# Kernel tuning notes

Measured on AMD Instinct MI355X. Metric: run time of the kernel, lower is better.

## Reference

```python
import jax, jax.numpy as jnp
import numpy as np

N, E = 4096, 4096          # nodes, hyperedges
IN_DIM, OUT_DIM, EDGE_DIM = 256, 256, 64
HEADS, DEG, CARD = 8, 8, 8  # node degree, edge cardinality (regular hypergraph)


def setup_inputs() -> dict:
    key = jax.random.key(0)
    ks = jax.random.split(key, 6)
    # regular hypergraph: DEG rounds, each a permutation of nodes chunked into
    # blocks of CARD -> every node in exactly DEG edges, every edge has CARD
    # distinct nodes. E = DEG * N / CARD.
    rng = np.random.default_rng(0)
    node_of_edge = np.concatenate(
        [rng.permutation(N).reshape(-1, CARD) for _ in range(DEG)], axis=0)  # [E, CARD]
    inc = np.zeros((E, N), dtype=np.float32)
    inc[np.arange(E)[:, None], node_of_edge] = 1.0
    s = 0.05
    return {
        "x": jax.random.normal(ks[0], (N, IN_DIM), jnp.float32),
        "incidence": jnp.asarray(inc),
        "edge_attr": jax.random.normal(ks[1], (E, EDGE_DIM), jnp.float32),
        "W_lin": jax.random.normal(ks[2], (IN_DIM, OUT_DIM), jnp.float32) * s,
        "W_edge": jax.random.normal(ks[3], (EDGE_DIM, OUT_DIM), jnp.float32) * s,
        "in_proj_w": jax.random.normal(ks[4], (3 * OUT_DIM, OUT_DIM), jnp.float32) * s,
        "in_proj_b": jnp.zeros((3 * OUT_DIM,), jnp.float32),
        "out_proj_w": jax.random.normal(ks[5], (OUT_DIM, OUT_DIM), jnp.float32) * s,
        "out_proj_b": jnp.zeros((OUT_DIM,), jnp.float32),
        "deg": DEG,
        "card": CARD,
    }


def reference(x, incidence, edge_attr, W_lin, W_edge,
              in_proj_w, in_proj_b, out_proj_w, out_proj_b, deg, card):
    n = x.shape[0]
    Wh = x @ W_lin          # [N, D]
    We = edge_attr @ W_edge  # [E, D]
    Dm = Wh.shape[1]
    H = HEADS
    dh = Dm // H
    # recover regular structure from the binary incidence matrix.
    # (attention is permutation-invariant over the pair set, so the order of
    #  indices returned by top_k vs torch.nonzero does not matter)
    _, edge_of_node = jax.lax.top_k(incidence.T, deg)   # [N, deg]
    _, node_of_edge = jax.lax.top_k(incidence, card)    # [E, card]
    pair_e = edge_of_node[:, :, None]                   # [N, deg, 1]
    pair_u = node_of_edge[edge_of_node]                 # [N, deg, card]
    L = deg * card
    Ksrc = (Wh[pair_u] + We[pair_e]).reshape(n, L, Dm)  # key source per pair
    Vsrc = Wh[pair_u].reshape(n, L, Dm)                 # value source per pair
    # torch nn.MultiheadAttention in/out projections
    Wq, Wk, Wv = jnp.split(in_proj_w, 3, axis=0)
    bq, bk, bv = jnp.split(in_proj_b, 3)
    q = (Wh @ Wq.T + bq).reshape(n, H, dh)              # q_len = 1 per node
    k = (Ksrc @ Wk.T + bk).reshape(n, L, H, dh)
    v = (Vsrc @ Wv.T + bv).reshape(n, L, H, dh)
    scale = 1.0 / jnp.sqrt(jnp.asarray(dh, q.dtype))
    scores = jnp.einsum('nhd,nlhd->nhl', q, k) * scale  # [N, H, L]
    attn = jax.nn.softmax(scores, axis=-1)
    ctx = jnp.einsum('nhl,nlhd->nhd', attn, v).reshape(n, Dm)
    out = ctx @ out_proj_w.T + out_proj_b
    return jax.nn.relu(out)
```

## Files before the change

### kernel.cpp

```cpp
#include <hip/hip_runtime.h>
#include <hip/hip_bf16.h>

#define NN    4096
#define EE    4096
#define DM    256
#define EDIM  64
#define HH    8
#define DHd   32
#define LL    64

typedef short  s16x8 __attribute__((ext_vector_type(8)));
typedef unsigned short u16x8 __attribute__((ext_vector_type(8)));
typedef float  f32x4 __attribute__((ext_vector_type(4)));
typedef unsigned int u32x4v __attribute__((ext_vector_type(4)));

#define SCALE 0.17677669529663687f

__device__ __forceinline__ float b2f(unsigned short u) {
  return __uint_as_float(((unsigned int)u) << 16);
}
__device__ __forceinline__ unsigned short f2b_bits(float f) {
  unsigned int u = __float_as_uint(f);
  u = (u + 0x7FFFu + ((u >> 16) & 1u)) >> 16;
  return (unsigned short)u;
}

#if __has_builtin(__builtin_amdgcn_fdot2_f32_bf16)
#define HAVE_DOT2B 1
typedef __bf16 bf2v __attribute__((ext_vector_type(2)));
__device__ __forceinline__ float dot2b(unsigned int a, unsigned int b, float c) {
  return __builtin_amdgcn_fdot2_f32_bf16(__builtin_bit_cast(bf2v, a),
                                         __builtin_bit_cast(bf2v, b), c, false);
}
#else
#define HAVE_DOT2B 0
#endif

#if __has_builtin(__builtin_amdgcn_update_dpp) && __has_builtin(__builtin_amdgcn_readfirstlane)
#define HAVE_DPP 1
template <int CTRL>
__device__ __forceinline__ float dpp_sum_step(float x) {
  int s = __builtin_amdgcn_update_dpp(0, __float_as_int(x), CTRL, 0xF, 0xF, true);
  return x + __int_as_float(s);
}
#else
#define HAVE_DPP 0
#endif

#define MODE_PLAIN 0
#define MODE_PROJ  1
#define MODE_OUT   2

__device__ __forceinline__ void gemm_mfma_body(
    short* As, short* Bs, f32x4 acc[2][2], int wr, int wc, int fr, int fk) {
  s16x8 af0 = *(const s16x8*)&As[(wr + fr) * 40 + fk];
  s16x8 af1 = *(const s16x8*)&As[(wr + 16 + fr) * 40 + fk];
  s16x8 bf0 = *(const s16x8*)&Bs[(wc + fr) * 40 + fk];
  s16x8 bf1 = *(const s16x8*)&Bs[(wc + 16 + fr) * 40 + fk];
  acc[0][0] = __builtin_amdgcn_mfma_f32_16x16x32_bf16(af0, bf0, acc[0][0], 0, 0, 0);
  acc[0][1] = __builtin_amdgcn_mfma_f32_16x16x32_bf16(af0, bf1, acc[0][1], 0, 0, 0);
  acc[1][0] = __builtin_amdgcn_mfma_f32_16x16x32_bf16(af1, bf0, acc[1][0], 0, 0, 0);
  acc[1][1] = __builtin_amdgcn_mfma_f32_16x16x32_bf16(af1, bf1, acc[1][1], 0, 0, 0);
}

__device__ __forceinline__ void gemm_tile(
    const unsigned short* __restrict__ A, const unsigned short* __restrict__ B,
    int i0, int j0, int N, int K, int mode,
    float* __restrict__ out_f, unsigned short* __restrict__ out_b,
    unsigned short* __restrict__ out_b2, const float* __restrict__ bias,
    short* As, short* Bs) {
  const int tid  = threadIdx.x;
  const int wid  = tid >> 6, lane = tid & 63;
  const int wr   = (wid >> 1) * 32, wc = (wid & 1) * 32;
  const int srow = tid >> 2, schunk = (tid & 3) * 8;
  const int fr   = lane & 15, fk = (lane >> 4) * 8;

  f32x4 acc[2][2];
#pragma unroll
  for (int a = 0; a < 2; ++a)
#pragma unroll
    for (int b = 0; b < 2; ++b) acc[a][b] = (f32x4){0.f, 0.f, 0.f, 0.f};

  for (int kk = 0; kk < K; kk += 32) {
    *(s16x8*)&As[srow * 40 + schunk] = *(const s16x8*)&A[(size_t)(i0 + srow) * K + kk + schunk];
    *(s16x8*)&Bs[srow * 40 + schunk] = *(const s16x8*)&B[(size_t)(j0 + srow) * K + kk + schunk];
    __syncthreads();
    gemm_mfma_body(As, Bs, acc, wr, wc, fr, fk);
    __syncthreads();
  }

  const int ecol = lane & 15, erow0 = (lane >> 4) * 4;
#pragma unroll
  for (int mi = 0; mi < 2; ++mi)
#pragma unroll
    for (int ni = 0; ni < 2; ++ni) {
#pragma unroll
      for (int v = 0; v < 4; ++v) {
        int i = i0 + wr + mi * 16 + erow0 + v;
        int j = j0 + wc + ni * 16 + ecol;
        float val = acc[mi][ni][v];
        if (mode == MODE_PLAIN) {
          out_b[(size_t)i * N + j] = f2b_bits(val);
        } else if (mode == MODE_PROJ) {
          if (j < 256)      out_b[(size_t)i * 256 + j]           = f2b_bits((val + bias[j]) * SCALE);
          else if (j < 512) out_b2[(size_t)i * 256 + (j - 256)]  = f2b_bits(val);
          else              ((unsigned short*)out_f)[(size_t)i * 256 + (j - 512)] = f2b_bits(val + bias[j]);
        } else {
          float r = val + bias[j];
          out_f[(size_t)i * N + j] = r > 0.f ? r : 0.f;
        }
      }
    }
}

__device__ __forceinline__ void gemm_tile_f32src(
    const float* __restrict__ A, const float* __restrict__ B,
    int i0, int j0, int N, int K,
    unsigned short* __restrict__ out_b, short* As, short* Bs) {
  const int tid  = threadIdx.x;
  const int wid  = tid >> 6, lane = tid & 63;
  const int wr   = (wid >> 1) * 32, wc = (wid & 1) * 32;
  const int srow = tid >> 2, schunk = (tid & 3) * 8;
  const int fr   = lane & 15, fk = (lane >> 4) * 8;

  f32x4 acc[2][2];
#pragma unroll
  for (int a = 0; a < 2; ++a)
#pragma unroll
    for (int b = 0; b < 2; ++b) acc[a][b] = (f32x4){0.f, 0.f, 0.f, 0.f};

  for (int kk = 0; kk < 256; kk += 32) {
    float4 a0 = *(const float4*)&A[(size_t)(i0 + srow) * 256 + kk + schunk];
    float4 a1 = *(const float4*)&A[(size_t)(i0 + srow) * 256 + kk + schunk + 4];
    float4 b0 = *(const float4*)&B[(size_t)(j0 + srow) * 256 + kk + schunk];
    float4 b1 = *(const float4*)&B[(size_t)(j0 + srow) * 256 + kk + schunk + 4];
    s16x8 av, bv;
    av[0] = (short)f2b_bits(a0.x); av[1] = (short)f2b_bits(a0.y);
    av[2] = (short)f2b_bits(a0.z); av[3] = (short)f2b_bits(a0.w);
    av[4] = (short)f2b_bits(a1.x); av[5] = (short)f2b_bits(a1.y);
    av[6] = (short)f2b_bits(a1.z); av[7] = (short)f2b_bits(a1.w);
    bv[0] = (short)f2b_bits(b0.x); bv[1] = (short)f2b_bits(b0.y);
    bv[2] = (short)f2b_bits(b0.z); bv[3] = (short)f2b_bits(b0.w);
    bv[4] = (short)f2b_bits(b1.x); bv[5] = (short)f2b_bits(b1.y);
    bv[6] = (short)f2b_bits(b1.z); bv[7] = (short)f2b_bits(b1.w);
    *(s16x8*)&As[srow * 40 + schunk] = av;
    *(s16x8*)&Bs[srow * 40 + schunk] = bv;
    __syncthreads();
    gemm_mfma_body(As, Bs, acc, wr, wc, fr, fk);
    __syncthreads();
  }

  const int ecol = lane & 15, erow0 = (lane >> 4) * 4;
#pragma unroll
  for (int mi = 0; mi < 2; ++mi)
#pragma unroll
    for (int ni = 0; ni < 2; ++ni)
#pragma unroll
      for (int v = 0; v < 4; ++v) {
        int i = i0 + wr + mi * 16 + erow0 + v;
        int j = j0 + wc + ni * 16 + ecol;
        if (j < N) out_b[(size_t)i * N + j] = f2b_bits(acc[mi][ni][v]);
      }
}

__device__ __forceinline__ void attn_head_math(
    const unsigned short* Klds, const unsigned short* Elds, float* Alds_wave,
    const u16x8 qstage[4], const u16x8 vstage[4],
    int h, int lane, int rg, int dchunk,
    unsigned short* __restrict__ ctx, size_t ctx_off) {
  const int kbase = lane * 512 + h * 64, ksw = (lane & 7) << 4;
  const int ebase = (lane >> 3) * 512 + h * 64, esw = ((lane >> 3) & 7) << 4;
  float s;
  {
    float s1 = 0.f, s2 = 0.f;
#pragma unroll
    for (int c = 0; c < 4; ++c) {
      u16x8 kv = *(const u16x8*)((const char*)Klds + ((kbase + c * 16) ^ ksw));
      u16x8 ev = *(const u16x8*)((const char*)Elds + ((ebase + c * 16) ^ esw));
      u16x8 qv = qstage[c];
#if HAVE_DOT2B
      u32x4v kw = __builtin_bit_cast(u32x4v, kv);
      u32x4v ew = __builtin_bit_cast(u32x4v, ev);
      u32x4v qw = __builtin_bit_cast(u32x4v, qv);
#pragma unroll
      for (int p = 0; p < 4; ++p) {
        s1 = dot2b(qw[p], kw[p], s1);
        s2 = dot2b(qw[p], ew[p], s2);
      }
#else
#pragma unroll
      for (int j = 0; j < 8; ++j)
        s1 += b2f(qv[j]) * (b2f(kv[j]) + b2f(ev[j]));
#endif
    }
    s = s1 + s2;
  }
  float p = __expf(s - 8.0f);
  float t = p + __shfl_xor(p, 16);
  t = t + __shfl_xor(t, 32);
#if HAVE_DPP
  t = dpp_sum_step<0x101>(t);
  t = dpp_sum_step<0x102>(t);
  t = dpp_sum_step<0x104>(t);
  t = dpp_sum_step<0x108>(t);
  float sum = __uint_as_float((unsigned)__builtin_amdgcn_readfirstlane(__float_as_int(t)));
#else
  t += __shfl_xor(t, 1); t += __shfl_xor(t, 2);
  t += __shfl_xor(t, 4); t += __shfl_xor(t, 8);
  float sum = t;
#endif
  const float a = __fdividef(p, sum);

  Alds_wave[lane] = a;
  float4 aq = *(const float4*)&Alds_wave[rg * 4];

  float acc[8];
#pragma unroll
  for (int j = 0; j < 8; ++j) acc[j] = 0.f;
#if HAVE_DOT2B
  {
    unsigned int pw01 = (unsigned int)f2b_bits(aq.x) | ((unsigned int)f2b_bits(aq.y) << 16);
    unsigned int pw23 = (unsigned int)f2b_bits(aq.z) | ((unsigned int)f2b_bits(aq.w) << 16);
    u32x4v v0 = __builtin_bit_cast(u32x4v, vstage[0]);
    u32x4v v1 = __builtin_bit_cast(u32x4v, vstage[1]);
    u32x4v v2 = __builtin_bit_cast(u32x4v, vstage[2]);
    u32x4v v3 = __builtin_bit_cast(u32x4v, vstage[3]);
#pragma unroll
    for (int jw = 0; jw < 4; ++jw) {
      unsigned int a01 = __builtin_amdgcn_perm(v1[jw], v0[jw], 0x05040100u);
      unsigned int b01 = __builtin_amdgcn_perm(v1[jw], v0[jw], 0x07060302u);
      unsigned int a23 = __builtin_amdgcn_perm(v3[jw], v2[jw], 0x05040100u);
      unsigned int b23 = __builtin_amdgcn_perm(v3[jw], v2[jw], 0x07060302u);
      acc[jw * 2]     = dot2b(pw01, a01, acc[jw * 2]);
      acc[jw * 2]     = dot2b(pw23, a23, acc[jw * 2]);
      acc[jw * 2 + 1] = dot2b(pw01, b01, acc[jw * 2 + 1]);
      acc[jw * 2 + 1] = dot2b(pw23, b23, acc[jw * 2 + 1]);
    }
  }
#else
#pragma unroll
  for (int i = 0; i < 4; ++i) {
    float pi = (i == 0) ? aq.x : (i == 1) ? aq.y : (i == 2) ? aq.z : aq.w;
#pragma unroll
    for (int j = 0; j < 8; ++j) acc[j] += pi * b2f(vstage[i][j]);
  }
#endif
#if HAVE_DPP
#pragma unroll
  for (int j = 0; j < 8; ++j) {
    acc[j] = dpp_sum_step<0x101>(acc[j]);
    acc[j] = dpp_sum_step<0x102>(acc[j]);
    acc[j] = dpp_sum_step<0x104>(acc[j]);
    acc[j] = dpp_sum_step<0x108>(acc[j]);
  }
#else
#pragma unroll
  for (int off = 1; off < 16; off <<= 1)
#pragma unroll
    for (int j = 0; j < 8; ++j) acc[j] += __shfl_xor(acc[j], off, 64);
#endif
  if (rg == 0) {
    u16x8 o;
#pragma unroll
    for (int j = 0; j < 8; ++j) o[j] = f2b_bits(acc[j]);
    *(u16x8*)(ctx + ctx_off + h * 32 + dchunk * 8) = o;
  }
}

#define MB_ ((size_t)1048576)
#define OFF_Q      ((size_t)0)
#define OFF_KN     (2*MB_)
#define OFF_VN     (4*MB_)
#define OFF_KE     (6*MB_)
#define OFF_CTX    (8*MB_)
#define OFF_XBF    (10*MB_)
#define OFF_EABF   (12*MB_)
#define OFF_WOUTBF (12*MB_+524288)
#define OFF_F      (13*MB_)
#define OFF_G      (13*MB_+524288)
#define OFF_PAIRU  (14*MB_)
#define OFF_CNTE   (15*MB_)
#define OFF_NOE    (15*MB_+32768)
#define OFF_EON    (15*MB_+163840)

__global__ __launch_bounds__(256) void mega1(
    const float* __restrict__ inc,
    int* __restrict__ cnt_e, int* __restrict__ cnt_n,
    int* __restrict__ noe, int* __restrict__ eon,
    const float* __restrict__ x, const float* __restrict__ ea,
    const float* __restrict__ wout,
    unsigned short* __restrict__ xb, unsigned short* __restrict__ eab,
    unsigned short* __restrict__ woutb,
    const float* __restrict__ ipw, const float* __restrict__ wlin,
    const float* __restrict__ wedge,
    unsigned short* __restrict__ F, unsigned short* __restrict__ G) {
  __shared__ short As[64 * 40] __attribute__((aligned(16)));
  __shared__ short Bs[64 * 40] __attribute__((aligned(16)));
  const int bid = blockIdx.x;
  if (bid < 16384) {
    int t = bid * 256 + threadIdx.x;
    float4 v = ((const float4*)inc)[t];
    int flat = t * 4;
    int e  = flat >> 12;
    int u0 = flat & 4095;
    float vals[4] = {v.x, v.y, v.z, v.w};
#pragma unroll
    for (int j = 0; j < 4; ++j) {
      if (vals[j] != 0.0f) {
        int u  = u0 + j;
        int pe = atomicAdd(&cnt_e[e], 1);
        noe[e * 8 + pe] = u;
        int pn = atomicAdd(&cnt_n[u], 1);
        eon[u * 8 + pn] = e;
      }
    }
    return;
  }
  if (bid < 17728) {
    int j = (bid - 16384) * 256 + threadIdx.x;
    const float* src; unsigned short* dst;
    if (j < 262144)      { src = x;    dst = xb; }
    else { j -= 262144;
    if (j < 65536)       { src = ea;   dst = eab; }
    else { j -= 65536;     src = wout; dst = woutb; } }
    float4 v = ((const float4*)src)[j];
    ushort4 o;
    o.x = f2b_bits(v.x); o.y = f2b_bits(v.y); o.z = f2b_bits(v.z); o.w = f2b_bits(v.w);
    ((ushort4*)dst)[j] = o;
    return;
  }
  int fb = bid - 17728;
  if (fb < 48) {
    gemm_tile_f32src(ipw, wlin, (fb >> 2) * 64, (fb & 3) * 64, 256, 256, F, As, Bs);
  } else {
    gemm_tile_f32src(ipw + 65536, wedge, (fb - 48) * 64, 0, 64, 256, G, As, Bs);
  }
}

__global__ __launch_bounds__(256) void mega2(
    const unsigned short* __restrict__ x_bf, const unsigned short* __restrict__ F,
    const unsigned short* __restrict__ ea_bf, const unsigned short* __restrict__ G,
    unsigned short* __restrict__ Q, unsigned short* __restrict__ Kn,
    unsigned short* __restrict__ Vn, unsigned short* __restrict__ Ke,
    const float* __restrict__ ipb,
    const int* __restrict__ eon, const int* __restrict__ noe,
    int* __restrict__ pair_u) {
  __shared__ short As[64 * 40] __attribute__((aligned(16)));
  __shared__ short Bs[64 * 40] __attribute__((aligned(16)));
  const int bid = blockIdx.x;
  if (bid < 768) {
    gemm_tile(x_bf, F, (bid & 63) * 64, (bid >> 6) * 64, 768, 256,
              MODE_PROJ, (float*)Vn, Q, Kn, ipb, As, Bs);
  } else if (bid < 1024) {
    int r = bid - 768;
    gemm_tile(ea_bf, G, (r & 63) * 64, (r >> 6) * 64, 256, 64,
              MODE_PLAIN, nullptr, Ke, nullptr, nullptr, As, Bs);
  } else {
    int wv = ((bid - 1024) * 256 + threadIdx.x) >> 6;
    int lane = threadIdx.x & 63;
#pragma unroll
    for (int r = 0; r < 16; ++r) {
      int n = wv * 16 + r;
      int e = eon[n * 8 + (lane >> 3)];
      pair_u[n * 64 + lane] = noe[e * 8 + (lane & 7)];
    }
  }
}

__global__ __launch_bounds__(512) void attn_kernel(
    const unsigned short* __restrict__ Q, const unsigned short* __restrict__ Kn,
    const unsigned short* __restrict__ Vn, const unsigned short* __restrict__ Ke,
    const int* __restrict__ eon, const int* __restrict__ pair_u,
    unsigned short* __restrict__ ctx) {
  __shared__ unsigned short Klds[64 * 256] __attribute__((aligned(16)));
  __shared__ unsigned short Elds[8 * 256]  __attribute__((aligned(16)));
  __shared__ float Alds[8 * 64];
  const int tid = threadIdx.x;
  const int h = tid >> 6, lane = tid & 63;
  const int rg = lane & 15, dchunk = lane >> 4;

  for (int it = 0; it < 4; ++it) {
    const int n = blockIdx.x * 4 + it;
    if (it) __syncthreads();

#pragma unroll
    for (int j = 0; j < 4; ++j) {
      int row = h * 8 + j * 2 + (lane >> 5);
      int u   = pair_u[n * 64 + row];
      u16x8 v = *(const u16x8*)(Kn + (size_t)u * 256 + (lane & 31) * 8);
      int db  = (row * 512 + (lane & 31) * 16) ^ ((row & 7) << 4);
      *(u16x8*)((char*)Klds + db) = v;
    }
    {
      int e = eon[n * 8 + h];
      if (lane < 32) {
        u16x8 v = *(const u16x8*)(Ke + (size_t)e * 256 + lane * 8);
        int db  = (h * 512 + lane * 16) ^ ((h & 7) << 4);
        *(u16x8*)((char*)Elds + db) = v;
      }
    }
    u16x8 vstage[4], qstage[4];
#pragma unroll
    for (int i = 0; i < 4; ++i) {
      int u = pair_u[n * 64 + rg * 4 + i];
      vstage[i] = *(const u16x8*)(Vn + (size_t)u * 256 + h * 32 + dchunk * 8);
    }
    {
      const u16x8* qp = (const u16x8*)(Q + (size_t)n * 256 + h * 32);
#pragma unroll
      for (int c = 0; c < 4; ++c) qstage[c] = qp[c];
    }
    __syncthreads();

    attn_head_math(Klds, Elds, &Alds[h << 6], qstage, vstage,
                   h, lane, rg, dchunk, ctx, (size_t)n * 256);
  }
}

__global__ __launch_bounds__(256) void gemm_out(
    const unsigned short* __restrict__ ctx, const unsigned short* __restrict__ wout_bf,
    float* __restrict__ out, const float* __restrict__ bias) {
  __shared__ short As[64 * 40] __attribute__((aligned(16)));
  __shared__ short Bs[64 * 40] __attribute__((aligned(16)));
  gemm_tile(ctx, wout_bf, blockIdx.x * 64, blockIdx.y * 64, 256, 256,
            MODE_OUT, out, nullptr, nullptr, bias, As, Bs);
}

extern "C" void kernel_launch(void* const* d_in, const int* in_sizes, int n_in,
                              void* d_out, int out_size, void* d_ws, size_t ws_size,
                              hipStream_t stream) {
  const float* x     = (const float*)d_in[0];
  const float* inc   = (const float*)d_in[1];
  const float* ea    = (const float*)d_in[2];
  const float* wlin  = (const float*)d_in[3];
  const float* wedge = (const float*)d_in[4];
  const float* ipw   = (const float*)d_in[5];
  const float* ipb   = (const float*)d_in[6];
  const float* wout  = (const float*)d_in[7];
  const float* outb  = (const float*)d_in[8];
  char* ws = (char*)d_ws;
  float* out = (float*)d_out;

  unsigned short* Q       = (unsigned short*)(ws + OFF_Q);
  unsigned short* Kn      = (unsigned short*)(ws + OFF_KN);
  unsigned short* Vn      = (unsigned short*)(ws + OFF_VN);
  unsigned short* Ke      = (unsigned short*)(ws + OFF_KE);
  unsigned short* ctx     = (unsigned short*)(ws + OFF_CTX);
  unsigned short* x_bf    = (unsigned short*)(ws + OFF_XBF);
  unsigned short* ea_bf   = (unsigned short*)(ws + OFF_EABF);
  unsigned short* wout_bf = (unsigned short*)(ws + OFF_WOUTBF);
  unsigned short* F       = (unsigned short*)(ws + OFF_F);
  unsigned short* G       = (unsigned short*)(ws + OFF_G);
  int*            cnt_e   = (int*)(ws + OFF_CNTE);
  int*            noe     = (int*)(ws + OFF_NOE);
  int*            eon     = (int*)(ws + OFF_EON);
  int*            pair_u  = (int*)(ws + OFF_PAIRU);

  hipMemsetAsync(ws + OFF_CNTE, 0, 32768, stream);

  mega1<<<17780, 256, 0, stream>>>(inc, cnt_e, (int*)(ws + OFF_CNTE) + 4096, noe, eon,
                                   x, ea, wout, x_bf, ea_bf, wout_bf,
                                   ipw, wlin, wedge, F, G);
  mega2<<<1088, 256, 0, stream>>>(x_bf, F, ea_bf, G, Q, Kn, Vn, Ke, ipb,
                                  eon, noe, pair_u);
  attn_kernel<<<1024, 512, 0, stream>>>(Q, Kn, Vn, Ke, eon, pair_u, ctx);
  gemm_out<<<dim3(64, 4), 256, 0, stream>>>(ctx, wout_bf, out, outb);
}
```

Before: 87.17 us.

## Process one node per attention block with waves handling two heads each

The attention kernel now launches one 256-thread block per node instead of 512-thread blocks looping over four nodes. Each wave stages K/E rows and handles two heads sequentially, reusing its softmax scratch. The aim is to drop the per-iteration block barriers and serialized node loop and to raise the number of resident blocks for latency hiding. In exchange each wave does twice the head math, and the per-node K gather is spread over fewer threads.

```diff
diff --git a/kernel.cpp b/kernel.cpp
--- a/kernel.cpp
+++ b/kernel.cpp
@@ -367,53 +367,53 @@
   }
 }
 
-__global__ __launch_bounds__(512) void attn_kernel(
+__global__ __launch_bounds__(256) void attn_kernel(
     const unsigned short* __restrict__ Q, const unsigned short* __restrict__ Kn,
     const unsigned short* __restrict__ Vn, const unsigned short* __restrict__ Ke,
     const int* __restrict__ eon, const int* __restrict__ pair_u,
     unsigned short* __restrict__ ctx) {
+  const int n = blockIdx.x;
   __shared__ unsigned short Klds[64 * 256] __attribute__((aligned(16)));
   __shared__ unsigned short Elds[8 * 256]  __attribute__((aligned(16)));
-  __shared__ float Alds[8 * 64];
+  __shared__ float Alds[4 * 64];
   const int tid = threadIdx.x;
-  const int h = tid >> 6, lane = tid & 63;
+  const int wid = tid >> 6, lane = tid & 63;
   const int rg = lane & 15, dchunk = lane >> 4;
 
-  for (int it = 0; it < 4; ++it) {
-    const int n = blockIdx.x * 4 + it;
-    if (it) __syncthreads();
-
-#pragma unroll
-    for (int j = 0; j < 4; ++j) {
-      int row = h * 8 + j * 2 + (lane >> 5);
-      int u   = pair_u[n * 64 + row];
-      u16x8 v = *(const u16x8*)(Kn + (size_t)u * 256 + (lane & 31) * 8);
-      int db  = (row * 512 + (lane & 31) * 16) ^ ((row & 7) << 4);
-      *(u16x8*)((char*)Klds + db) = v;
-    }
-    {
-      int e = eon[n * 8 + h];
-      if (lane < 32) {
-        u16x8 v = *(const u16x8*)(Ke + (size_t)e * 256 + lane * 8);
-        int db  = (h * 512 + lane * 16) ^ ((h & 7) << 4);
-        *(u16x8*)((char*)Elds + db) = v;
-      }
-    }
-    u16x8 vstage[4], qstage[4];
+#pragma unroll
+  for (int j = 0; j < 8; ++j) {
+    int row = wid * 16 + j * 2 + (lane >> 5);
+    int u   = pair_u[n * 64 + row];
+    u16x8 v = *(const u16x8*)(Kn + (size_t)u * 256 + (lane & 31) * 8);
+    int db  = (row * 512 + (lane & 31) * 16) ^ ((row & 7) << 4);
+    *(u16x8*)((char*)Klds + db) = v;
+  }
+  {
+    int row = wid * 2 + (lane >> 5);
+    int e   = eon[n * 8 + row];
+    u16x8 v = *(const u16x8*)(Ke + (size_t)e * 256 + (lane & 31) * 8);
+    int db  = (row * 512 + (lane & 31) * 16) ^ ((row & 7) << 4);
+    *(u16x8*)((char*)Elds + db) = v;
+  }
+  u16x8 vstage[2][4], qstage[2][4];
+#pragma unroll
+  for (int hp = 0; hp < 2; ++hp) {
+    const int h = wid * 2 + hp;
 #pragma unroll
     for (int i = 0; i < 4; ++i) {
       int u = pair_u[n * 64 + rg * 4 + i];
-      vstage[i] = *(const u16x8*)(Vn + (size_t)u * 256 + h * 32 + dchunk * 8);
-    }
-    {
-      const u16x8* qp = (const u16x8*)(Q + (size_t)n * 256 + h * 32);
-#pragma unroll
-      for (int c = 0; c < 4; ++c) qstage[c] = qp[c];
-    }
-    __syncthreads();
-
-    attn_head_math(Klds, Elds, &Alds[h << 6], qstage, vstage,
-                   h, lane, rg, dchunk, ctx, (size_t)n * 256);
+      vstage[hp][i] = *(const u16x8*)(Vn + (size_t)u * 256 + h * 32 + dchunk * 8);
+    }
+    const u16x8* qp = (const u16x8*)(Q + (size_t)n * 256 + h * 32);
+#pragma unroll
+    for (int c = 0; c < 4; ++c) qstage[hp][c] = qp[c];
+  }
+  __syncthreads();
+
+#pragma unroll
+  for (int hp = 0; hp < 2; ++hp) {
+    attn_head_math(Klds, Elds, &Alds[wid << 6], qstage[hp], vstage[hp],
+                   wid * 2 + hp, lane, rg, dchunk, ctx, (size_t)n * 256);
   }
 }
 
@@ -463,6 +463,6 @@
                                    ipw, wlin, wedge, F, G);
   mega2<<<1088, 256, 0, stream>>>(x_bf, F, ea_bf, G, Q, Kn, Vn, Ke, ipb,
                                   eon, noe, pair_u);
-  attn_kernel<<<1024, 512, 0, stream>>>(Q, Kn, Vn, Ke, eon, pair_u, ctx);
+  attn_kernel<<<4096, 256, 0, stream>>>(Q, Kn, Vn, Ke, eon, pair_u, ctx);
   gemm_out<<<dim3(64, 4), 256, 0, stream>>>(ctx, wout_bf, out, outb);
 }
```

Result: faster. 80.48 us (median of 2 runs) (-7.7%).

## Double-buffer attention K/E staging to overlap gathers with head math

Applied to the files above, without the earlier changes.

The attention kernel's four-node loop is unrolled by hand, and the key and edge-key LDS buffers are double-buffered. The gather for node i+1 (K/E rows into LDS, V/Q into registers) is issued before the attention math for node i, hiding global-memory latency behind compute. The cost is double the LDS footprint and two extra register stage sets. A launch-bounds occupancy hint is also added, which may cap registers and cause spills.

```diff
diff --git a/kernel.cpp b/kernel.cpp
--- a/kernel.cpp
+++ b/kernel.cpp
@@ -367,54 +367,80 @@
   }
 }
 
-__global__ __launch_bounds__(512) void attn_kernel(
+__global__ __launch_bounds__(512, 4) void attn_kernel(
     const unsigned short* __restrict__ Q, const unsigned short* __restrict__ Kn,
     const unsigned short* __restrict__ Vn, const unsigned short* __restrict__ Ke,
     const int* __restrict__ eon, const int* __restrict__ pair_u,
     unsigned short* __restrict__ ctx) {
-  __shared__ unsigned short Klds[64 * 256] __attribute__((aligned(16)));
-  __shared__ unsigned short Elds[8 * 256]  __attribute__((aligned(16)));
+  __shared__ unsigned short Klds[2][64 * 256] __attribute__((aligned(16)));
+  __shared__ unsigned short Elds[2][8 * 256]  __attribute__((aligned(16)));
   __shared__ float Alds[8 * 64];
   const int tid = threadIdx.x;
   const int h = tid >> 6, lane = tid & 63;
   const int rg = lane & 15, dchunk = lane >> 4;
-
-  for (int it = 0; it < 4; ++it) {
-    const int n = blockIdx.x * 4 + it;
-    if (it) __syncthreads();
-
-#pragma unroll
-    for (int j = 0; j < 4; ++j) {
-      int row = h * 8 + j * 2 + (lane >> 5);
-      int u   = pair_u[n * 64 + row];
-      u16x8 v = *(const u16x8*)(Kn + (size_t)u * 256 + (lane & 31) * 8);
-      int db  = (row * 512 + (lane & 31) * 16) ^ ((row & 7) << 4);
-      *(u16x8*)((char*)Klds + db) = v;
-    }
-    {
-      int e = eon[n * 8 + h];
-      if (lane < 32) {
-        u16x8 v = *(const u16x8*)(Ke + (size_t)e * 256 + lane * 8);
-        int db  = (h * 512 + lane * 16) ^ ((h & 7) << 4);
-        *(u16x8*)((char*)Elds + db) = v;
-      }
-    }
-    u16x8 vstage[4], qstage[4];
-#pragma unroll
-    for (int i = 0; i < 4; ++i) {
-      int u = pair_u[n * 64 + rg * 4 + i];
-      vstage[i] = *(const u16x8*)(Vn + (size_t)u * 256 + h * 32 + dchunk * 8);
-    }
-    {
-      const u16x8* qp = (const u16x8*)(Q + (size_t)n * 256 + h * 32);
-#pragma unroll
-      for (int c = 0; c < 4; ++c) qstage[c] = qp[c];
-    }
-    __syncthreads();
-
-    attn_head_math(Klds, Elds, &Alds[h << 6], qstage, vstage,
-                   h, lane, rg, dchunk, ctx, (size_t)n * 256);
-  }
+  const int n0 = blockIdx.x * 4;
+
+#define STAGE_KE(buf, n)                                                       \
+  {                                                                            \
+    _Pragma("unroll")                                                          \
+    for (int j = 0; j < 4; ++j) {                                              \
+      int row = h * 8 + j * 2 + (lane >> 5);                                   \
+      int u   = pair_u[(n) * 64 + row];                                        \
+      u16x8 v = *(const u16x8*)(Kn + (size_t)u * 256 + (lane & 31) * 8);       \
+      int db  = (row * 512 + (lane & 31) * 16) ^ ((row & 7) << 4);             \
+      *(u16x8*)((char*)Klds[buf] + db) = v;                                    \
+    }                                                                          \
+    {                                                                          \
+      int e = eon[(n) * 8 + h];                                                \
+      if (lane < 32) {                                                         \
+        u16x8 v = *(const u16x8*)(Ke + (size_t)e * 256 + lane * 8);            \
+        int db  = (h * 512 + lane * 16) ^ ((h & 7) << 4);                      \
+        *(u16x8*)((char*)Elds[buf] + db) = v;                                  \
+      }                                                                        \
+    }                                                                          \
+  }
+
+#define LOAD_VQ(vs, qs, n)                                                     \
+  {                                                                            \
+    _Pragma("unroll")                                                          \
+    for (int i = 0; i < 4; ++i) {                                              \
+      int u = pair_u[(n) * 64 + rg * 4 + i];                                   \
+      vs[i] = *(const u16x8*)(Vn + (size_t)u * 256 + h * 32 + dchunk * 8);     \
+    }                                                                          \
+    const u16x8* qp = (const u16x8*)(Q + (size_t)(n) * 256 + h * 32);          \
+    _Pragma("unroll")                                                          \
+    for (int c = 0; c < 4; ++c) qs[c] = qp[c];                                 \
+  }
+
+  u16x8 vA[4], qA[4], vB[4], qB[4];
+
+  STAGE_KE(0, n0);
+  LOAD_VQ(vA, qA, n0);
+  __syncthreads();
+
+  STAGE_KE(1, n0 + 1);
+  LOAD_VQ(vB, qB, n0 + 1);
+  attn_head_math(Klds[0], Elds[0], &Alds[h << 6], qA, vA,
+                 h, lane, rg, dchunk, ctx, (size_t)n0 * 256);
+  __syncthreads();
+
+  STAGE_KE(0, n0 + 2);
+  LOAD_VQ(vA, qA, n0 + 2);
+  attn_head_math(Klds[1], Elds[1], &Alds[h << 6], qB, vB,
+                 h, lane, rg, dchunk, ctx, (size_t)(n0 + 1) * 256);
+  __syncthreads();
+
+  STAGE_KE(1, n0 + 3);
+  LOAD_VQ(vB, qB, n0 + 3);
+  attn_head_math(Klds[0], Elds[0], &Alds[h << 6], qA, vA,
+                 h, lane, rg, dchunk, ctx, (size_t)(n0 + 2) * 256);
+  __syncthreads();
+
+  attn_head_math(Klds[1], Elds[1], &Alds[h << 6], qB, vB,
+                 h, lane, rg, dchunk, ctx, (size_t)(n0 + 3) * 256);
+
+#undef STAGE_KE
+#undef LOAD_VQ
 }
 
 __global__ __launch_bounds__(256) void gemm_out(
```

Result: no change. 86.49 us (-0.8%).
